# Optimization experiments

Hardware: AMD Instinct MI355X
Metric: run time of the kernel (lower is better)

Reference implementation:

```python
import jax, jax.numpy as jnp
import numpy as np

S, B, D = 4096, 4, 1024
APERTURE = 256
SCALE = 1.0 / np.sqrt(D)
EPS = 1e-6
NEG_INF = -jnp.inf


def _xavier(key, shape, gain=np.sqrt(2.0)):
    fan_in, fan_out = shape[1], shape[0]
    a = gain * np.sqrt(6.0 / (fan_in + fan_out))
    return jax.random.uniform(key, shape, jnp.float32, -a, a)


def setup_inputs() -> dict:
    key = jax.random.key(0)
    ks = jax.random.split(key, 8)
    return {
        "x": jax.random.normal(ks[0], (S, B, D), jnp.float32),
        "Wk": _xavier(ks[1], (D, D)),
        "Wq": _xavier(ks[2], (D, D)),
        "Wv": _xavier(ks[3], (D, D)),
        "Wp": _xavier(ks[4], (D, D)),
        "W1": _xavier(ks[5], (D, D)),
        "b1": jnp.full((D,), 0.1, jnp.float32),
        "W2": _xavier(ks[6], (1, D)),
        "b2": jnp.full((1,), 0.1, jnp.float32),
        "gamma": jnp.ones((D,), jnp.float32),
        "beta": jnp.zeros((D,), jnp.float32),
    }


def _layer_norm(y, gamma, beta):
    m = jnp.mean(y, axis=-1, keepdims=True)
    v = jnp.mean((y - m) ** 2, axis=-1, keepdims=True)
    return (y - m) * jax.lax.rsqrt(v + EPS) * gamma + beta


def reference(x, Wk, Wq, Wv, Wp, W1, b1, W2, b2, gamma, beta):
    # x: (S, B, D) -> (B, S, D)
    xb = jnp.transpose(x, (1, 0, 2))
    K = jnp.einsum('bsd,ed->bse', xb, Wk)
    Q = jnp.einsum('bsd,ed->bse', xb, Wq)
    V = jnp.einsum('bsd,ed->bse', xb, Wv)
    e = jnp.einsum('bqd,bkd->bqk', Q, K) * SCALE  # (B, S, S)
    # ignore_self: -inf on diagonal
    eye = jnp.eye(S, dtype=bool)
    e = jnp.where(eye[None, :, :], NEG_INF, e)
    # aperture mask: torch masks where tril(e,ap)*triu(e,-ap) == 0
    scope = jnp.tril(e, APERTURE) * jnp.triu(e, -APERTURE)
    e = jnp.where(scope == 0, NEG_INF, e)
    alpha = jax.nn.softmax(e, axis=2)  # dropout is identity at eval
    c = jnp.einsum('bqk,bkd->bqd', alpha, V)
    c = jnp.einsum('bqd,ed->bqe', c, Wp)
    y = c + xb
    y = _layer_norm(y, gamma, beta)
    y = jax.nn.relu(jnp.einsum('bsd,ed->bse', y, W1) + b1)
    y = _layer_norm(y, gamma, beta)
    y = jax.nn.sigmoid(jnp.einsum('bsd,ed->bse', y, W2) + b2)  # (B, S, 1)
    return jnp.transpose(y, (1, 0, 2))  # (S, B, 1)
```

## Files before the change

### kernel.cpp

```cpp
#include <hip/hip_runtime.h>
#include <stdint.h>
#include <math.h>

#define S_LEN 4096
#define BATCH 4
#define DIM   1024
#define AP    256
#define NBLK  32
#define BANDC 640
#define SCALE 0.03125f

typedef __attribute__((ext_vector_type(4))) float f32x4;
typedef __attribute__((ext_vector_type(8))) short bf16x8;

__device__ __forceinline__ ushort f2bf(float f) {
  union { float f; uint32_t u; } v; v.f = f;
  uint32_t r = v.u + 0x7FFFu + ((v.u >> 16) & 1u);
  return (ushort)(r >> 16);
}

__device__ __forceinline__ void gload16(const void* g, void* l) {
  __builtin_amdgcn_global_load_lds((const __attribute__((address_space(1))) void*)g,
                                   (__attribute__((address_space(3))) void*)l,
                                   16, 0, 0);
}

__device__ __forceinline__ float block_sum(float v, float* red) {
  #pragma unroll
  for (int o = 32; o > 0; o >>= 1) v += __shfl_xor(v, o, 64);
  const int w = threadIdx.x >> 6;
  if ((threadIdx.x & 63) == 0) red[w] = v;
  __syncthreads();
  v = red[0] + red[1] + red[2] + red[3];
  __syncthreads();
  return v;
}

__device__ __forceinline__ float block_max(float v, float* red) {
  #pragma unroll
  for (int o = 32; o > 0; o >>= 1) v = fmaxf(v, __shfl_xor(v, o, 64));
  const int w = threadIdx.x >> 6;
  if ((threadIdx.x & 63) == 0) red[w] = v;
  __syncthreads();
  v = fmaxf(fmaxf(red[0], red[1]), fmaxf(red[2], red[3]));
  __syncthreads();
  return v;
}

#define STAGE2(dstbase, g0, g1, kcol) \
  gload16((g0) + (kcol), lds + (dstbase) + stOff); \
  gload16((g1) + (kcol), lds + (dstbase) + 4096 + stOff);

#define MFMA_QUAD(arow, bvec) \
  _Pragma("unroll") for (int m = 0; m < 4; ++m) \
  _Pragma("unroll") for (int n = 0; n < 4; ++n) \
    acc[(arow) + m][n] = __builtin_amdgcn_mfma_f32_16x16x32_bf16(a[m], bvec[n], acc[(arow) + m][n], 0, 0, 0);

#define PHASE_TAIL() \
  __builtin_amdgcn_s_barrier(); \
  asm volatile("s_waitcnt lgkmcnt(0)" ::: "memory"); \
  __builtin_amdgcn_sched_barrier(0); \
  __builtin_amdgcn_s_setprio(1);

#define PHASE_END() \
  __builtin_amdgcn_s_setprio(0); \
  __builtin_amdgcn_sched_barrier(0); \
  __builtin_amdgcn_s_barrier();

__device__ __forceinline__ void gemm256_core(
    const ushort* __restrict__ Ablk, int lda,
    const ushort* __restrict__ Bblk, int ldb,
    int K, ushort* __restrict__ lds,
    f32x4 acc[8][4])
{
  const int tid  = threadIdx.x;
  const int lane = tid & 63;
  const int wave = tid >> 6;
  const int wr = wave >> 2;
  const int wn = wave & 3;

  const int srow = tid >> 2;
  const int gseg = (tid & 3) ^ ((tid >> 3) & 3);
  const ushort* gA0 = Ablk + (size_t)srow * lda + gseg * 8;
  const ushort* gA1 = Ablk + (size_t)(srow + 128) * lda + gseg * 8;
  const ushort* gB0 = Bblk + (size_t)srow * ldb + gseg * 8;
  const ushort* gB1 = Bblk + (size_t)(srow + 128) * ldb + gseg * 8;
  const int stOff = wave * 512;

  const int l15 = lane & 15;
  const int seg = (lane >> 4) ^ ((lane >> 1) & 3);
  const int raBase = (wr * 128 + l15) * 32 + seg * 8;
  const int rbBase = (wn * 64  + l15) * 32 + seg * 8;

  const int NT = K >> 6;

  STAGE2(0,     gA0, gA1, 0)
  STAGE2(16384, gB0, gB1, 0)
  STAGE2(8192,  gA0, gA1, 32)
  STAGE2(24576, gB0, gB1, 32)
  asm volatile("s_waitcnt vmcnt(4)" ::: "memory");
  __builtin_amdgcn_s_barrier();

  for (int t = 0; t < NT; ++t) {
    const int rb = (t & 1) * 32768;
    const int sb = ((t + 1) & 1) * 32768;
    const int k1 = (t + 1) << 6;
    const bool more = (t + 1 < NT);

    bf16x8 a[4], b0[4], b1[4];

    #pragma unroll
    for (int m = 0; m < 4; ++m) a[m] = *(const bf16x8*)(lds + rb + raBase + m * 512);
    #pragma unroll
    for (int n = 0; n < 4; ++n) b0[n] = *(const bf16x8*)(lds + rb + 16384 + rbBase + n * 512);
    if (more) { STAGE2(sb, gA0, gA1, k1) }
    PHASE_TAIL()
    MFMA_QUAD(0, b0)
    PHASE_END()

    #pragma unroll
    for (int m = 0; m < 4; ++m) a[m] = *(const bf16x8*)(lds + rb + raBase + (m + 4) * 512);
    if (more) {
      STAGE2(sb + 16384, gB0, gB1, k1)
      asm volatile("s_waitcnt vmcnt(4)" ::: "memory");
    } else {
      asm volatile("s_waitcnt vmcnt(0)" ::: "memory");
    }
    PHASE_TAIL()
    MFMA_QUAD(4, b0)
    PHASE_END()

    #pragma unroll
    for (int m = 0; m < 4; ++m) a[m] = *(const bf16x8*)(lds + rb + 8192 + raBase + m * 512);
    #pragma unroll
    for (int n = 0; n < 4; ++n) b1[n] = *(const bf16x8*)(lds + rb + 24576 + rbBase + n * 512);
    if (more) { STAGE2(sb + 8192, gA0, gA1, k1 + 32) }
    PHASE_TAIL()
    MFMA_QUAD(0, b1)
    PHASE_END()

    #pragma unroll
    for (int m = 0; m < 4; ++m) a[m] = *(const bf16x8*)(lds + rb + 8192 + raBase + (m + 4) * 512);
    if (more) {
      STAGE2(sb + 24576, gB0, gB1, k1 + 32)
      asm volatile("s_waitcnt vmcnt(4)" ::: "memory");
    }
    PHASE_TAIL()
    MFMA_QUAD(4, b1)
    PHASE_END()
  }
}

#define ACC256_ZERO(acc) \
  _Pragma("unroll") for (int m_ = 0; m_ < 8; m_++) \
  _Pragma("unroll") for (int n_ = 0; n_ < 4; n_++) \
  _Pragma("unroll") for (int r_ = 0; r_ < 4; r_++) acc[m_][n_][r_] = 0.0f;

#define EPI256_BEGIN(acc) { \
  const int lane_ = threadIdx.x & 63; \
  const int wave_ = threadIdx.x >> 6; \
  const int wrb_ = (wave_ >> 2) * 128; \
  const int wnb_ = (wave_ & 3) * 64; \
  const int rb_ = (lane_ >> 4) << 2; \
  const int cb_ = lane_ & 15; \
  _Pragma("unroll") for (int m_ = 0; m_ < 8; m_++) \
  _Pragma("unroll") for (int n_ = 0; n_ < 4; n_++) \
  _Pragma("unroll") for (int r_ = 0; r_ < 4; r_++) { \
    const int rloc = wrb_ + m_ * 16 + rb_ + r_; \
    const int cloc = wnb_ + n_ * 16 + cb_; \
    const float aval = acc[m_][n_][r_];
#define EPI256_END() } }

__device__ __forceinline__ void gemm_core(
    const ushort* __restrict__ Ablk, int lda,
    const ushort* __restrict__ Bblk, int ldb,
    int k_begin, int k_end,
    ushort* __restrict__ lds,
    f32x4 acc[4][4])
{
  const int tid  = threadIdx.x;
  const int lane = tid & 63;
  const int wr = ((tid >> 7) & 1) * 64;
  const int wc = ((tid >> 6) & 1) * 64;
  const int lr = lane & 15;
  const int seg = (lane >> 4) ^ ((lane >> 1) & 3);

  const int srow = tid >> 2;
  const int gseg = (tid & 3) ^ ((tid >> 3) & 3);
  const ushort* gA0 = Ablk + (size_t)srow * lda + gseg * 8;
  const ushort* gA1 = Ablk + (size_t)(srow + 64) * lda + gseg * 8;
  const ushort* gB0 = Bblk + (size_t)srow * ldb + gseg * 8;
  const ushort* gB1 = Bblk + (size_t)(srow + 64) * ldb + gseg * 8;
  const int stA = (tid >> 6) * 512;

  const int NT = (k_end - k_begin) >> 5;

  gload16(gA0 + k_begin, lds + stA);
  gload16(gA1 + k_begin, lds + 2048 + stA);
  gload16(gB0 + k_begin, lds + 4096 + stA);
  gload16(gB1 + k_begin, lds + 6144 + stA);

  for (int t = 0; t < NT; ++t) {
    if (t + 1 < NT) {
      ushort* buf = lds + ((t + 1) & 1) * 8192;
      const int k0 = k_begin + (t + 1) * 32;
      gload16(gA0 + k0, buf + stA);
      gload16(gA1 + k0, buf + 2048 + stA);
      gload16(gB0 + k0, buf + 4096 + stA);
      gload16(gB1 + k0, buf + 6144 + stA);
      asm volatile("s_waitcnt vmcnt(4)" ::: "memory");
    } else {
      asm volatile("s_waitcnt vmcnt(0)" ::: "memory");
    }
    __builtin_amdgcn_s_barrier();

    const ushort* buf = lds + (t & 1) * 8192;
    bf16x8 af[4], bfv[4];
    #pragma unroll
    for (int m = 0; m < 4; m++)
      af[m] = *(const bf16x8*)(buf + (wr + m * 16 + lr) * 32 + seg * 8);
    #pragma unroll
    for (int n = 0; n < 4; n++)
      bfv[n] = *(const bf16x8*)(buf + 4096 + (wc + n * 16 + lr) * 32 + seg * 8);

    __builtin_amdgcn_s_setprio(1);
    #pragma unroll
    for (int m = 0; m < 4; m++)
      #pragma unroll
      for (int n = 0; n < 4; n++)
        acc[m][n] = __builtin_amdgcn_mfma_f32_16x16x32_bf16(af[m], bfv[n], acc[m][n], 0, 0, 0);
    __builtin_amdgcn_s_setprio(0);
    asm volatile("s_waitcnt lgkmcnt(0)" ::: "memory");
  }
}

#define ACC_ZERO(acc) \
  _Pragma("unroll") for (int m_ = 0; m_ < 4; m_++) \
  _Pragma("unroll") for (int n_ = 0; n_ < 4; n_++) \
  _Pragma("unroll") for (int r_ = 0; r_ < 4; r_++) acc[m_][n_][r_] = 0.0f;

#define EPI_BEGIN(acc) { \
  const int lane_ = threadIdx.x & 63; \
  const int wr_ = ((threadIdx.x >> 7) & 1) * 64; \
  const int wc_ = ((threadIdx.x >> 6) & 1) * 64; \
  const int rb_ = (lane_ >> 4) << 2; \
  const int cb_ = lane_ & 15; \
  _Pragma("unroll") for (int m_ = 0; m_ < 4; m_++) \
  _Pragma("unroll") for (int n_ = 0; n_ < 4; n_++) \
  _Pragma("unroll") for (int r_ = 0; r_ < 4; r_++) { \
    const int rloc = wr_ + m_ * 16 + rb_ + r_; \
    const int cloc = wc_ + n_ * 16 + cb_; \
    const float aval = acc[m_][n_][r_];
#define EPI_END() } }

__global__ __launch_bounds__(256) void prep_x(const float* __restrict__ x, ushort* __restrict__ xb) {
  size_t idx = ((size_t)blockIdx.x * 256 + threadIdx.x) * 4;
  int d = (int)(idx & 1023);
  int s = (int)((idx >> 10) & 4095);
  int b = (int)(idx >> 22);
  float4 v = *(const float4*)(x + ((size_t)s * BATCH + b) * DIM + d);
  ushort4 o;
  o.x = f2bf(v.x); o.y = f2bf(v.y); o.z = f2bf(v.z); o.w = f2bf(v.w);
  *(ushort4*)(xb + idx) = o;
}

__global__ __launch_bounds__(256) void f2bf_vec(const float* __restrict__ src, ushort* __restrict__ dst, int n) {
  int idx = (blockIdx.x * 256 + threadIdx.x) * 4;
  if (idx >= n) return;
  float4 v = *(const float4*)(src + idx);
  ushort4 o;
  o.x = f2bf(v.x); o.y = f2bf(v.y); o.z = f2bf(v.z); o.w = f2bf(v.w);
  *(ushort4*)(dst + idx) = o;
}

__global__ __launch_bounds__(512, 2) void qkv_gemm256(
    const ushort* __restrict__ xb, const ushort* __restrict__ wqkv,
    ushort* __restrict__ Kp, ushort* __restrict__ Qp, ushort* __restrict__ Vp)
{
  __shared__ ushort lds[65536];
  const int nid = (blockIdx.x & 7) * 96 + (blockIdx.x >> 3);
  const int by = nid / 12;
  const int bx = nid % 12;
  f32x4 acc[8][4];
  ACC256_ZERO(acc)
  gemm256_core(xb + (size_t)by * 256 * DIM, DIM,
               wqkv + (size_t)bx * 256 * DIM, DIM, DIM, lds, acc);
  ushort* dst = (bx < 4) ? Kp : (bx < 8) ? Qp : Vp;
  const int colb = (bx & 3) * 256;
  EPI256_BEGIN(acc)
    int row = by * 256 + rloc;
    int col = colb + cloc;
    dst[(size_t)row * DIM + col] = f2bf(aval);
  EPI256_END()
}

__global__ __launch_bounds__(512, 2) void wp_gemm256(
    const ushort* __restrict__ cbuf, const ushort* __restrict__ wpb,
    const float* __restrict__ x, float* __restrict__ y0)
{
  __shared__ ushort lds[65536];
  const int nid = (blockIdx.x & 7) * 32 + (blockIdx.x >> 3);
  const int by = nid >> 2;
  const int bx = nid & 3;
  f32x4 acc[8][4];
  ACC256_ZERO(acc)
  gemm256_core(cbuf + (size_t)by * 256 * DIM, DIM,
               wpb + (size_t)bx * 256 * DIM, DIM, DIM, lds, acc);
  EPI256_BEGIN(acc)
    int row = by * 256 + rloc;
    int col = bx * 256 + cloc;
    int b = row >> 12, s = row & 4095;
    y0[(size_t)row * DIM + col] = aval + x[((size_t)s * BATCH + b) * DIM + col];
  EPI256_END()
}

__global__ __launch_bounds__(512, 2) void ffn1_gemm256(
    const ushort* __restrict__ y1, const ushort* __restrict__ w1b,
    const float* __restrict__ b1, float* __restrict__ h0)
{
  __shared__ ushort lds[65536];
  const int nid = (blockIdx.x & 7) * 32 + (blockIdx.x >> 3);
  const int by = nid >> 2;
  const int bx = nid & 3;
  f32x4 acc[8][4];
  ACC256_ZERO(acc)
  gemm256_core(y1 + (size_t)by * 256 * DIM, DIM,
               w1b + (size_t)bx * 256 * DIM, DIM, DIM, lds, acc);
  EPI256_BEGIN(acc)
    int row = by * 256 + rloc;
    int col = bx * 256 + cloc;
    h0[(size_t)row * DIM + col] = fmaxf(aval + b1[col], 0.0f);
  EPI256_END()
}

__global__ __launch_bounds__(256) void transpose_v(const ushort* __restrict__ V, ushort* __restrict__ VT) {
  __shared__ ushort tile[64][66];
  const int s0 = blockIdx.x * 64, d0 = blockIdx.y * 64, b = blockIdx.z;
  const ushort* Vb = V + (size_t)b * S_LEN * DIM;
  ushort* VTb = VT + (size_t)b * DIM * S_LEN;
  #pragma unroll
  for (int it = 0; it < 16; it++) {
    int flat = it * 256 + threadIdx.x;
    int r = flat >> 6, c = flat & 63;
    tile[r][c] = Vb[(size_t)(s0 + r) * DIM + d0 + c];
  }
  __syncthreads();
  #pragma unroll
  for (int it = 0; it < 16; it++) {
    int flat = it * 256 + threadIdx.x;
    int r = flat >> 6, c = flat & 63;
    VTb[(size_t)(d0 + r) * S_LEN + s0 + c] = tile[c][r];
  }
}

__global__ __launch_bounds__(256) void scores_gemm(
    const ushort* __restrict__ Qp, const ushort* __restrict__ Kp,
    float* __restrict__ eband)
{
  const int nid = (blockIdx.x & 7) * 80 + (blockIdx.x >> 3);
  const int b   = nid / 160;
  const int rem = nid % 160;
  const int i   = rem / 5;
  const int jj  = rem % 5;
  const int j   = i - 2 + jj;
  if (j < 0 || j >= NBLK) return;
  __shared__ ushort lds[16384];
  f32x4 acc[4][4];
  ACC_ZERO(acc)
  gemm_core(Qp + ((size_t)b * S_LEN + i * 128) * DIM, DIM,
            Kp + ((size_t)b * S_LEN + j * 128) * DIM, DIM, 0, DIM, lds, acc);
  EPI_BEGIN(acc)
    int q = i * 128 + rloc;
    int k = j * 128 + cloc;
    float v = aval * SCALE;
    int dqk = q - k;
    if (dqk == 0 || dqk > AP || dqk < -AP) v = -INFINITY;
    eband[((size_t)b * S_LEN + q) * BANDC + jj * 128 + cloc] = v;
  EPI_END()
}

__global__ __launch_bounds__(256) void softmax_band(const float* __restrict__ eband,
                                                    ushort* __restrict__ aband)
{
  __shared__ float red[4];
  const int qg = blockIdx.x;
  const int s  = qg & 4095;
  const int i  = s >> 7;
  const float* row = eband + (size_t)qg * BANDC;
  ushort* arow = aband + (size_t)qg * BANDC;

  float vals[3];
  bool  valid[3];
  float mx = -INFINITY;
  #pragma unroll
  for (int t = 0; t < 3; t++) {
    int idx = threadIdx.x + t * 256;
    int jj = idx >> 7;
    int j = i - 2 + jj;
    bool ok = (idx < BANDC) && (j >= 0) && (j < NBLK);
    valid[t] = ok;
    float v = ok ? row[idx] : -INFINITY;
    vals[t] = v;
    mx = fmaxf(mx, v);
  }
  float bmax = block_max(mx, red);
  float ss = 0.0f;
  #pragma unroll
  for (int t = 0; t < 3; t++) {
    float e = valid[t] ? __expf(vals[t] - bmax) : 0.0f;
    vals[t] = e;
    ss += e;
  }
  float inv = 1.0f / block_sum(ss, red);
  #pragma unroll
  for (int t = 0; t < 3; t++) {
    int idx = threadIdx.x + t * 256;
    if (idx < BANDC) arow[idx] = f2bf(vals[t] * inv);
  }
}

__global__ __launch_bounds__(256) void av_gemm(
    const ushort* __restrict__ aband, const ushort* __restrict__ VT,
    ushort* __restrict__ cbuf)
{
  const int nid = (blockIdx.x & 7) * 128 + (blockIdx.x >> 3);
  const int by = nid >> 3;
  const int b = by >> 5, i = by & 31;
  const int bx = nid & 7;
  const int jj_lo = (i < 2) ? (2 - i) : 0;
  const int jj_hi = (i > 29) ? (34 - i) : 5;
  __shared__ ushort lds[16384];
  f32x4 acc[4][4];
  ACC_ZERO(acc)
  const ushort* Ablk = aband + ((size_t)b * S_LEN + i * 128) * BANDC;
  const ushort* Bblk = VT + (size_t)b * DIM * S_LEN + (size_t)bx * 128 * S_LEN + (i - 2) * 128;
  gemm_core(Ablk, BANDC, Bblk, S_LEN, jj_lo * 128, jj_hi * 128, lds, acc);
  EPI_BEGIN(acc)
    int row = b * S_LEN + i * 128 + rloc;
    int col = bx * 128 + cloc;
    cbuf[(size_t)row * DIM + col] = f2bf(aval);
  EPI_END()
}

__global__ __launch_bounds__(256) void ln_kernel(const float* __restrict__ y0, ushort* __restrict__ y1,
                                                 const float* __restrict__ gamma, const float* __restrict__ beta)
{
  __shared__ float red[4];
  const size_t q = blockIdx.x;
  const float* row = y0 + q * DIM;
  float v[4];
  #pragma unroll
  for (int t = 0; t < 4; t++) v[t] = row[threadIdx.x + t * 256];
  float mean = block_sum(v[0] + v[1] + v[2] + v[3], red) * (1.0f / DIM);
  float q2 = 0.0f;
  #pragma unroll
  for (int t = 0; t < 4; t++) { float d = v[t] - mean; q2 += d * d; }
  float var = block_sum(q2, red) * (1.0f / DIM);
  float rstd = rsqrtf(var + 1e-6f);
  #pragma unroll
  for (int t = 0; t < 4; t++) {
    int d = threadIdx.x + t * 256;
    y1[q * DIM + d] = f2bf((v[t] - mean) * rstd * gamma[d] + beta[d]);
  }
}

__global__ __launch_bounds__(256) void head_kernel(const float* __restrict__ h0,
    const float* __restrict__ gamma, const float* __restrict__ beta,
    const float* __restrict__ W2, const float* __restrict__ b2,
    float* __restrict__ out)
{
  __shared__ float red[4];
  const int qg = blockIdx.x;
  const int b = qg >> 12, s = qg & 4095;
  const float* row = h0 + (size_t)qg * DIM;
  float v[4];
  #pragma unroll
  for (int t = 0; t < 4; t++) v[t] = row[threadIdx.x + t * 256];
  float mean = block_sum(v[0] + v[1] + v[2] + v[3], red) * (1.0f / DIM);
  float q2 = 0.0f;
  #pragma unroll
  for (int t = 0; t < 4; t++) { float d = v[t] - mean; q2 += d * d; }
  float var = block_sum(q2, red) * (1.0f / DIM);
  float rstd = rsqrtf(var + 1e-6f);
  float part = 0.0f;
  #pragma unroll
  for (int t = 0; t < 4; t++) {
    int d = threadIdx.x + t * 256;
    part += ((v[t] - mean) * rstd * gamma[d] + beta[d]) * W2[d];
  }
  float logit = block_sum(part, red) + b2[0];
  if (threadIdx.x == 0) out[(size_t)s * BATCH + b] = 1.0f / (1.0f + expf(-logit));
}

extern "C" void kernel_launch(void* const* d_in, const int* in_sizes, int n_in,
                              void* d_out, int out_size, void* d_ws, size_t ws_size,
                              hipStream_t stream) {
  const float* x     = (const float*)d_in[0];
  const float* Wk    = (const float*)d_in[1];
  const float* Wq    = (const float*)d_in[2];
  const float* Wv    = (const float*)d_in[3];
  const float* Wp    = (const float*)d_in[4];
  const float* W1    = (const float*)d_in[5];
  const float* b1    = (const float*)d_in[6];
  const float* W2    = (const float*)d_in[7];
  const float* b2    = (const float*)d_in[8];
  const float* gamma = (const float*)d_in[9];
  const float* beta  = (const float*)d_in[10];
  float* out = (float*)d_out;

  char* w = (char*)d_ws;
  ushort* xb   = (ushort*)(w + 0);
  ushort* wqkv = (ushort*)(w + 33554432);
  ushort* wpb  = (ushort*)(w + 39845888);
  ushort* w1b  = (ushort*)(w + 41943040);
  ushort* Qp   = (ushort*)(w + 44040192);
  ushort* Kp   = (ushort*)(w + 77594624);
  ushort* Vp   = (ushort*)(w + 111149056);
  ushort* VT   = (ushort*)(w + 144703488);
  float*  big  = (float*)(w + 178257920);
  ushort* aband = Qp;
  ushort* cbuf  = Kp;
  ushort* y1    = Vp;
  float* eband = big;
  float* y0    = big;
  float* h0    = big;

  prep_x<<<16384, 256, 0, stream>>>(x, xb);
  f2bf_vec<<<1024, 256, 0, stream>>>(Wk, wqkv,            1048576);
  f2bf_vec<<<1024, 256, 0, stream>>>(Wq, wqkv + 1048576,  1048576);
  f2bf_vec<<<1024, 256, 0, stream>>>(Wv, wqkv + 2097152,  1048576);
  f2bf_vec<<<1024, 256, 0, stream>>>(Wp, wpb, 1048576);
  f2bf_vec<<<1024, 256, 0, stream>>>(W1, w1b, 1048576);

  qkv_gemm256<<<768, 512, 0, stream>>>(xb, wqkv, Kp, Qp, Vp);
  transpose_v<<<dim3(64, 16, 4), 256, 0, stream>>>(Vp, VT);
  scores_gemm<<<640, 256, 0, stream>>>(Qp, Kp, eband);
  softmax_band<<<16384, 256, 0, stream>>>(eband, aband);
  av_gemm<<<1024, 256, 0, stream>>>(aband, VT, cbuf);
  wp_gemm256<<<256, 512, 0, stream>>>(cbuf, wpb, x, y0);
  ln_kernel<<<16384, 256, 0, stream>>>(y0, y1, gamma, beta);
  ffn1_gemm256<<<256, 512, 0, stream>>>(y1, w1b, b1, h0);
  head_kernel<<<16384, 256, 0, stream>>>(h0, gamma, beta, W2, b2, out);
}
```

Before: 383.4 us.

## Stage GEMM epilogues through LDS for coalesced stores, merge weight casts, drop sched barriers

The qkv and av GEMM epilogues now write bf16 results into swizzled LDS and then emit 16-byte coalesced global stores, replacing scattered 2-byte stores. The five weight-conversion launches are merged into one kernel to cut launch overhead. The sched_barrier fences around the MFMA phases are removed, so the compiler may reorder across phase boundaries. This adds LDS traffic and extra block syncs in the epilogues, and removing the fences could disturb the hand-tuned pipeline.

New measurement: 377.5 us. No clear change (-1.5%).

```diff
diff --git a/kernel.cpp b/kernel.cpp
--- a/kernel.cpp
+++ b/kernel.cpp
@@ -59,12 +59,10 @@
 #define PHASE_TAIL() \
   __builtin_amdgcn_s_barrier(); \
   asm volatile("s_waitcnt lgkmcnt(0)" ::: "memory"); \
-  __builtin_amdgcn_sched_barrier(0); \
   __builtin_amdgcn_s_setprio(1);
 
 #define PHASE_END() \
   __builtin_amdgcn_s_setprio(0); \
-  __builtin_amdgcn_sched_barrier(0); \
   __builtin_amdgcn_s_barrier();
 
 __device__ __forceinline__ void gemm256_core(
@@ -155,6 +153,40 @@
   _Pragma("unroll") for (int m_ = 0; m_ < 8; m_++) \
   _Pragma("unroll") for (int n_ = 0; n_ < 4; n_++) \
   _Pragma("unroll") for (int r_ = 0; r_ < 4; r_++) acc[m_][n_][r_] = 0.0f;
+
+__device__ __forceinline__ void epi256_store_bf16(
+    f32x4 acc[8][4], ushort* __restrict__ lds,
+    ushort* __restrict__ dst, int rowbase, int colb)
+{
+  __syncthreads();
+  const int lane_ = threadIdx.x & 63;
+  const int wave_ = threadIdx.x >> 6;
+  const int wrb_ = (wave_ >> 2) * 128;
+  const int wnb_ = (wave_ & 3) * 64;
+  const int rb_ = (lane_ >> 4) << 2;
+  const int cb_ = lane_ & 15;
+  #pragma unroll
+  for (int m = 0; m < 8; m++)
+    #pragma unroll
+    for (int n = 0; n < 4; n++)
+      #pragma unroll
+      for (int r = 0; r < 4; r++) {
+        const int rl = wrb_ + m * 16 + rb_ + r;
+        const int cl = wnb_ + n * 16 + cb_;
+        const int cs = cl ^ (((rl >> 2) & 3) << 4);
+        lds[rl * 256 + cs] = f2bf(acc[m][n][r]);
+      }
+  __syncthreads();
+  #pragma unroll
+  for (int it = 0; it < 16; ++it) {
+    const int chunk = it * 512 + threadIdx.x;
+    const int rl = chunk >> 5;
+    const int c16 = chunk & 31;
+    const int csw = (c16 * 16) ^ (((rl >> 2) & 3) << 5);
+    bf16x8 v = *(const bf16x8*)((const char*)lds + rl * 512 + csw);
+    *(bf16x8*)(dst + (size_t)(rowbase + rl) * DIM + colb + c16 * 8) = v;
+  }
+}
 
 #define EPI256_BEGIN(acc) { \
   const int lane_ = threadIdx.x & 63; \
@@ -264,9 +296,18 @@
   *(ushort4*)(xb + idx) = o;
 }
 
-__global__ __launch_bounds__(256) void f2bf_vec(const float* __restrict__ src, ushort* __restrict__ dst, int n) {
-  int idx = (blockIdx.x * 256 + threadIdx.x) * 4;
-  if (idx >= n) return;
+__global__ __launch_bounds__(256) void f2bf_all(
+    const float* __restrict__ Wk, const float* __restrict__ Wq, const float* __restrict__ Wv,
+    const float* __restrict__ Wp, const float* __restrict__ W1,
+    ushort* __restrict__ wqkv, ushort* __restrict__ wpb, ushort* __restrict__ w1b)
+{
+  const int g = blockIdx.x;
+  const int which = g >> 10;
+  const int idx = ((g & 1023) * 256 + threadIdx.x) * 4;
+  const float* src = (which == 0) ? Wk : (which == 1) ? Wq : (which == 2) ? Wv
+                   : (which == 3) ? Wp : W1;
+  ushort* dst = (which == 0) ? wqkv : (which == 1) ? wqkv + 1048576
+              : (which == 2) ? wqkv + 2097152 : (which == 3) ? wpb : w1b;
   float4 v = *(const float4*)(src + idx);
   ushort4 o;
   o.x = f2bf(v.x); o.y = f2bf(v.y); o.z = f2bf(v.z); o.w = f2bf(v.w);
@@ -286,12 +327,7 @@
   gemm256_core(xb + (size_t)by * 256 * DIM, DIM,
                wqkv + (size_t)bx * 256 * DIM, DIM, DIM, lds, acc);
   ushort* dst = (bx < 4) ? Kp : (bx < 8) ? Qp : Vp;
-  const int colb = (bx & 3) * 256;
-  EPI256_BEGIN(acc)
-    int row = by * 256 + rloc;
-    int col = colb + cloc;
-    dst[(size_t)row * DIM + col] = f2bf(aval);
-  EPI256_END()
+  epi256_store_bf16(acc, lds, dst, by * 256, (bx & 3) * 256);
 }
 
 __global__ __launch_bounds__(512, 2) void wp_gemm256(
@@ -435,11 +471,37 @@
   const ushort* Ablk = aband + ((size_t)b * S_LEN + i * 128) * BANDC;
   const ushort* Bblk = VT + (size_t)b * DIM * S_LEN + (size_t)bx * 128 * S_LEN + (i - 2) * 128;
   gemm_core(Ablk, BANDC, Bblk, S_LEN, jj_lo * 128, jj_hi * 128, lds, acc);
-  EPI_BEGIN(acc)
-    int row = b * S_LEN + i * 128 + rloc;
-    int col = bx * 128 + cloc;
-    cbuf[(size_t)row * DIM + col] = f2bf(aval);
-  EPI_END()
+
+  __syncthreads();
+  {
+    const int lane_ = threadIdx.x & 63;
+    const int wr_ = ((threadIdx.x >> 7) & 1) * 64;
+    const int wc_ = ((threadIdx.x >> 6) & 1) * 64;
+    const int rb_ = (lane_ >> 4) << 2;
+    const int cb_ = lane_ & 15;
+    #pragma unroll
+    for (int m = 0; m < 4; m++)
+      #pragma unroll
+      for (int n = 0; n < 4; n++)
+        #pragma unroll
+        for (int r = 0; r < 4; r++) {
+          const int rl = wr_ + m * 16 + rb_ + r;
+          const int cl = wc_ + n * 16 + cb_;
+          const int cs = cl ^ (((rl >> 2) & 3) << 4);
+          lds[rl * 128 + cs] = f2bf(acc[m][n][r]);
+        }
+  }
+  __syncthreads();
+  ushort* dst = cbuf + ((size_t)b * S_LEN + i * 128) * DIM + bx * 128;
+  #pragma unroll
+  for (int it = 0; it < 8; ++it) {
+    const int chunk = it * 256 + threadIdx.x;
+    const int rl = chunk >> 4;
+    const int c16 = chunk & 15;
+    const int csw = (c16 * 16) ^ (((rl >> 2) & 3) << 5);
+    bf16x8 v = *(const bf16x8*)((const char*)lds + rl * 256 + csw);
+    *(bf16x8*)(dst + (size_t)rl * DIM + c16 * 8) = v;
+  }
 }
 
 __global__ __launch_bounds__(256) void ln_kernel(const float* __restrict__ y0, ushort* __restrict__ y1,
@@ -526,11 +588,7 @@
   float* h0    = big;
 
   prep_x<<<16384, 256, 0, stream>>>(x, xb);
-  f2bf_vec<<<1024, 256, 0, stream>>>(Wk, wqkv,            1048576);
-  f2bf_vec<<<1024, 256, 0, stream>>>(Wq, wqkv + 1048576,  1048576);
-  f2bf_vec<<<1024, 256, 0, stream>>>(Wv, wqkv + 2097152,  1048576);
-  f2bf_vec<<<1024, 256, 0, stream>>>(Wp, wpb, 1048576);
-  f2bf_vec<<<1024, 256, 0, stream>>>(W1, w1b, 1048576);
+  f2bf_all<<<5120, 256, 0, stream>>>(Wk, Wq, Wv, Wp, W1, wqkv, wpb, w1b);
 
   qkv_gemm256<<<768, 512, 0, stream>>>(xb, wqkv, Kp, Qp, Vp);
   transpose_v<<<dim3(64, 16, 4), 256, 0, stream>>>(Vp, VT);
```
